# Performance work log

Measured on AMD Instinct MI355X. Metric: run time of the kernel, lower is better.

Reference implementation:

```python
import jax, jax.numpy as jnp
import numpy as np

FEAT_STRIDE = 16
PRE_NMS_TOPN = 6000
POST_NMS_TOPN = 300
NMS_THRESH = 0.7
NEG = -1e9  # sentinel for suppressed scores


def generate_anchors(base_size=16, ratios=np.array([0.5, 1.0, 2.0]), scales=np.array([8.0, 16.0, 32.0])):
    ctr = (base_size - 1) / 2.0
    size = float(base_size * base_size)
    ws_r = np.round(np.sqrt(size / ratios))
    hs_r = np.round(ws_r * ratios)
    ws = (ws_r[:, None] * scales[None, :]).reshape(-1)
    hs = (hs_r[:, None] * scales[None, :]).reshape(-1)
    return np.stack([ctr - 0.5 * (ws - 1), ctr - 0.5 * (hs - 1),
                     ctr + 0.5 * (ws - 1), ctr + 0.5 * (hs - 1)], axis=1).astype(np.float32)

ANCHORS = jnp.asarray(generate_anchors())  # [A, 4]


def bbox_transform_inv(anchors, deltas):
    # anchors [N,4], deltas [B,N,4] -> [B,N,4]
    w = anchors[:, 2] - anchors[:, 0] + 1.0
    h = anchors[:, 3] - anchors[:, 1] + 1.0
    cx = anchors[:, 0] + 0.5 * w
    cy = anchors[:, 1] + 0.5 * h
    dx, dy, dw, dh = deltas[..., 0], deltas[..., 1], deltas[..., 2], deltas[..., 3]
    pcx = dx * w + cx
    pcy = dy * h + cy
    pw = jnp.exp(dw) * w
    ph = jnp.exp(dh) * h
    return jnp.stack([pcx - 0.5 * pw, pcy - 0.5 * ph, pcx + 0.5 * pw, pcy + 0.5 * ph], axis=-1)


def nms_single(boxes, scores):
    # Greedy NMS on pre-sorted candidates; boxes [N,4], scores [N].
    areas = (boxes[:, 2] - boxes[:, 0] + 1.0) * (boxes[:, 3] - boxes[:, 1] + 1.0)

    def body(sc, _):
        i = jnp.argmax(sc)
        valid = sc[i] > NEG / 2
        b = boxes[i]
        xx1 = jnp.maximum(b[0], boxes[:, 0])
        yy1 = jnp.maximum(b[1], boxes[:, 1])
        xx2 = jnp.minimum(b[2], boxes[:, 2])
        yy2 = jnp.minimum(b[3], boxes[:, 3])
        inter = jnp.maximum(xx2 - xx1 + 1.0, 0.0) * jnp.maximum(yy2 - yy1 + 1.0, 0.0)
        iou = inter / (areas[i] + areas - inter)
        sc = jnp.where(iou > NMS_THRESH, NEG, sc)  # suppress (includes self, iou=1)
        return sc, (i, valid)

    _, (keep, valid) = jax.lax.scan(body, scores, None, length=POST_NMS_TOPN)
    kept_boxes = jnp.where(valid[:, None], boxes[keep], 0.0)  # pad rows -> zeros
    return kept_boxes


def reference(scores, bbox_deltas, im_info):
    B, _, H, W = scores.shape
    A = ANCHORS.shape[0]
    # fg probs: second set of A channels -> [B, K*A]
    fg = jnp.transpose(scores[:, A:, :, :], (0, 2, 3, 1)).reshape(B, -1)
    deltas = jnp.transpose(bbox_deltas, (0, 2, 3, 1)).reshape(B, -1, 4)

    # Shifted anchors over the feature grid: [K*A, 4]
    sx = jnp.arange(W, dtype=jnp.float32) * FEAT_STRIDE
    sy = jnp.arange(H, dtype=jnp.float32) * FEAT_STRIDE
    mx, my = jnp.meshgrid(sx, sy)  # [H, W]
    shifts = jnp.stack([mx.ravel(), my.ravel(), mx.ravel(), my.ravel()], axis=1)  # [K,4]
    anchors = (ANCHORS[None, :, :] + shifts[:, None, :]).reshape(-1, 4)

    proposals = bbox_transform_inv(anchors, deltas)  # [B, K*A, 4]

    # Clip to image per batch element (im_info = [height, width, scale])
    wmax = (im_info[:, 1] - 1.0)[:, None]
    hmax = (im_info[:, 0] - 1.0)[:, None]
    proposals = jnp.stack([
        jnp.clip(proposals[..., 0], 0.0, wmax),
        jnp.clip(proposals[..., 1], 0.0, hmax),
        jnp.clip(proposals[..., 2], 0.0, wmax),
        jnp.clip(proposals[..., 3], 0.0, hmax)], axis=-1)

    # Top pre_nms_topN by score (sorted descending)
    top_scores, top_idx = jax.lax.top_k(fg, PRE_NMS_TOPN)            # [B, pre]
    top_boxes = jnp.take_along_axis(proposals, top_idx[..., None], axis=1)  # [B, pre, 4]

    kept = jax.vmap(nms_single)(top_boxes, top_scores)  # [B, post, 4]

    batch_col = jnp.broadcast_to(
        jnp.arange(B, dtype=kept.dtype)[:, None, None], (B, POST_NMS_TOPN, 1))
    return jnp.concatenate([batch_col, kept], axis=-1)  # [B, post, 5]


def setup_inputs() -> dict:
    key = jax.random.key(0)
    k1, k2 = jax.random.split(key)
    B, A, H, W = 16, 9, 192, 192
    scores = jax.random.uniform(k1, (B, 2 * A, H, W), dtype=jnp.float32)
    bbox_deltas = jax.random.normal(k2, (B, 4 * A, H, W), dtype=jnp.float32) * 0.5
    im_info = jnp.tile(jnp.array([[H * 16.0, W * 16.0, 1.0]], dtype=jnp.float32), (B, 1))
    return {"scores": scores, "bbox_deltas": bbox_deltas, "im_info": im_info}
```

## Files before the change

kernel.cpp:

```cpp
#include <hip/hip_runtime.h>
#include <stdint.h>

#define A_NUM    9
#define W_FEAT   192
#define H_FEAT   192
#define K_FEAT   (W_FEAT * H_FEAT)
#define N_ANCH   (K_FEAT * A_NUM)
#define BATCH    16
#define PRE_NMS  6000
#define POST_NMS 300
#define CAP      8192
#define CHUNK    4096
#define BPB      (N_ANCH / CHUNK)
#define CPA      (K_FEAT / CHUNK)
#define SORT2    2048
#define NWORD    (SORT2 / 64)
#define SLOTS    64

#define T2KEY    0xBF7Fu

typedef unsigned long long u64;

__constant__ float c_anchors[A_NUM][4] = {
    { -84.f,  -40.f,  99.f,  55.f},
    {-176.f,  -88.f, 191.f, 103.f},
    {-360.f, -184.f, 375.f, 199.f},
    { -56.f,  -56.f,  71.f,  71.f},
    {-120.f, -120.f, 135.f, 135.f},
    {-248.f, -248.f, 263.f, 263.f},
    { -36.f,  -80.f,  51.f,  95.f},
    { -80.f, -168.f,  95.f, 183.f},
    {-168.f, -344.f, 183.f, 359.f},
};

__device__ __forceinline__ unsigned key_bits(float s) {
    unsigned ub = __float_as_uint(s);
    return (ub & 0x80000000u) ? ~ub : (ub | 0x80000000u);
}

__device__ __forceinline__ const float* chunk_ptr(const float* scores, int blk,
                                                  int& b, int& a, int& koff) {
    b = blk / BPB;
    int chunk = blk - b * BPB;
    a = chunk / CPA;
    koff = (chunk - a * CPA) * CHUNK;
    return scores + ((size_t)(b * 2 * A_NUM + A_NUM + a)) * K_FEAT + koff;
}

__device__ __forceinline__ void hist_add(unsigned* lh, unsigned bin) {
    unsigned long long peers = __ballot(1);
// ... 18 lines not shown
    float dh = deltas[dbase + (size_t)3 * K_FEAT];
    float ax1 = c_anchors[a][0] + ww * 16.0f;
    float ay1 = c_anchors[a][1] + hh * 16.0f;
    float ax2 = c_anchors[a][2] + ww * 16.0f;
    float ay2 = c_anchors[a][3] + hh * 16.0f;
    float waf = ax2 - ax1 + 1.0f, haf = ay2 - ay1 + 1.0f;
    float cx = ax1 + 0.5f * waf, cy = ay1 + 0.5f * haf;
    float pcx = dx * waf + cx, pcy = dy * haf + cy;
    float pw = expf(dw) * waf, ph = expf(dh) * haf;
    float4 box;
    box.x = fminf(fmaxf(pcx - 0.5f * pw, 0.f), wmax);
    box.y = fminf(fmaxf(pcy - 0.5f * ph, 0.f), hmax);
    box.z = fminf(fmaxf(pcx + 0.5f * pw, 0.f), wmax);
    box.w = fminf(fmaxf(pcy + 0.5f * ph, 0.f), hmax);
    return box;
}

__device__ __forceinline__ bool iou_over(float4 a, float aa, float4 c, float ca) {
    float xx1 = fmaxf(a.x, c.x), yy1 = fmaxf(a.y, c.y);
    float xx2 = fminf(a.z, c.z), yy2 = fminf(a.w, c.w);
    float iw = fmaxf(xx2 - xx1 + 1.f, 0.f);
    float ih = fmaxf(yy2 - yy1 + 1.f, 0.f);
    float inter = iw * ih;
    return inter > 0.7f * (aa + ca - inter);
}

__device__ __forceinline__ u64 shflxor64(u64 v, int j) {
    unsigned lo = (unsigned)v, hi = (unsigned)(v >> 32);
    lo = __shfl_xor(lo, j, 64);
    hi = __shfl_xor(hi, j, 64);
    return ((u64)hi << 32) | lo;
}

__global__ __launch_bounds__(256) void compact_kernel(
        const float* __restrict__ scores,
        unsigned* __restrict__ cnt_blk,
        u64* __restrict__ cand) {
    __shared__ u64 sbuf[256];
    __shared__ unsigned scount;
    int tid = threadIdx.x;
    if (tid == 0) scount = 0;
    __syncthreads();
    int b, a, koff;
    const float* p = chunk_ptr(scores, blockIdx.x, b, a, koff);
    const float4* p4 = (const float4*)p;
    #pragma unroll
    for (int it = 0; it < CHUNK / 1024; ++it) {
        float4 v = p4[it * 256 + tid];
        unsigned e0 = (unsigned)(koff + (it * 256 + tid) * 4);
        float vv[4] = {v.x, v.y, v.z, v.w};
        #pragma unroll
        for (int j = 0; j < 4; ++j) {
            unsigned ub = key_bits(vv[j]);
            if ((ub >> 16) >= T2KEY) {
                unsigned n = (e0 + j) * A_NUM + a;
                unsigned pos = atomicAdd(&scount, 1u);
                if (pos < 256)
                    sbuf[pos] = ((u64)ub << 32) | (unsigned)(~n);
            }
        }
    }
    __syncthreads();
    unsigned c = scount;
    if (tid == 0) cnt_blk[blockIdx.x] = c;
    unsigned cw = c < SLOTS ? c : SLOTS;
    if (tid < cw) cand[(size_t)blockIdx.x * SLOTS + tid] = sbuf[tid];
}

#define KEYRD(I)  ((((u64)khi[(I)]) << 32) | klo[(I)])
#define KEYWR(I, V) do { khi[(I)] = (unsigned)((V) >> 32); klo[(I)] = (unsigned)(V); } while (0)

#define CE_SHFL(E, J, DESC) do { \
    u64 _v = shflxor64((E), (J)); \
    bool _kmax = ((DESC) == ((l & (J)) == 0)); \
    (E) = _kmax ? ((E) > _v ? (E) : _v) : ((E) < _v ? (E) : _v); \
} while (0)

#define CE_PAIR(A, B, DESC) do { \
    u64 _mx = (A) > (B) ? (A) : (B); \
    u64 _mn = (A) > (B) ? (B) : (A); \
    if (DESC) { (A) = _mx; (B) = _mn; } else { (A) = _mn; (B) = _mx; } \
} while (0)

#define LDS_PHASE(K, J) do { \
    _Pragma("unroll") \
    for (int pp = 0; pp < 2; ++pp) { \
        unsigned p = (unsigned)tid + (unsigned)pp * 512u; \
        unsigned i = ((p & ~((unsigned)(J) - 1u)) << 1) | (p & ((unsigned)(J) - 1u)); \
        unsigned ixj = i | (unsigned)(J); \
        u64 x = KEYRD(i), y = KEYRD(ixj); \
        bool dsc = ((i & (unsigned)(K)) == 0u); \
        if (dsc ? (x < y) : (x > y)) { KEYWR(i, y); KEYWR(ixj, x); } \
    } \
    __syncthreads(); \
} while (0)

#define REG_TAIL(D) do { \
    int seg = w << 8; \
    bool d = (D); \
    u64 e0 = KEYRD(seg + l); \
    u64 e1 = KEYRD(seg + 64 + l); \
    u64 e2 = KEYRD(seg + 128 + l); \
    u64 e3 = KEYRD(seg + 192 + l); \
    CE_PAIR(e0, e2, d); CE_PAIR(e1, e3, d); \
    CE_PAIR(e0, e1, d); CE_PAIR(e2, e3, d); \
    _Pragma("unroll") \
    for (int j = 32; j >= 1; j >>= 1) { \
        CE_SHFL(e0, j, d); CE_SHFL(e1, j, d); \
        CE_SHFL(e2, j, d); CE_SHFL(e3, j, d); \
    } \
    KEYWR(seg + l, e0); KEYWR(seg + 64 + l, e1); \
    KEYWR(seg + 128 + l, e2); KEYWR(seg + 192 + l, e3); \
    __syncthreads(); \
} while (0)

__global__ __launch_bounds__(512) void sort_kernel(
        const unsigned* __restrict__ cnt_blk,
        const u64* __restrict__ cand,
        const float* __restrict__ deltas,
        const float* __restrict__ im_info,
        float4* __restrict__ bxg,
        unsigned* __restrict__ m2arr,
        unsigned* __restrict__ okarr) {
    int b = blockIdx.x;
    __shared__ unsigned khi[SORT2];
    __shared__ unsigned klo[SORT2];
    __shared__ unsigned offs[BPB + 1];
    __shared__ unsigned ovfl;
    int tid = threadIdx.x;
    int l = tid & 63, w = tid >> 6;

    if (tid == 0) { ovfl = 0; offs[0] = 0; }
    __syncthreads();
    if (tid < BPB) {
        unsigned c = cnt_blk[b * BPB + tid];
        if (c > SLOTS) atomicOr(&ovfl, 1u);
        offs[tid + 1] = (c > SLOTS) ? SLOTS : c;
    }
    for (int i = tid; i < SORT2; i += 512) { khi[i] = 0u; klo[i] = 0u; }
    __syncthreads();
    if (tid == 0)
        for (int i = 1; i <= BPB; ++i) offs[i] += offs[i - 1];
    __syncthreads();
    unsigned m2 = offs[BPB];
    bool ok = (!ovfl) && (m2 >= 1) && (m2 <= SORT2);

    if (ok) {
        for (int s = w; s < BPB; s += 8) {
            unsigned c = offs[s + 1] - offs[s];
            if ((unsigned)l < c) {
                u64 k = cand[(size_t)(b * BPB + s) * SLOTS + l];
                KEYWR(offs[s] + l, k);
            }
        }
    }
    __syncthreads();

    if (ok) {
        {
            int seg = w << 8;
            u64 e0 = KEYRD(seg + l);
            u64 e1 = KEYRD(seg + 64 + l);
            u64 e2 = KEYRD(seg + 128 + l);
            u64 e3 = KEYRD(seg + 192 + l);
            #pragma unroll
            for (int k = 2; k <= 32; k <<= 1) {
                bool d = ((l & k) == 0);
                #pragma unroll
                for (int j = k >> 1; j >= 1; j >>= 1) {
                    CE_SHFL(e0, j, d); CE_SHFL(e1, j, d);
                    CE_SHFL(e2, j, d); CE_SHFL(e3, j, d);
                }
            }
            #pragma unroll
            for (int j = 32; j >= 1; j >>= 1) {
                CE_SHFL(e0, j, true);  CE_SHFL(e1, j, false);
                CE_SHFL(e2, j, true);  CE_SHFL(e3, j, false);
            }
            CE_PAIR(e0, e1, true); CE_PAIR(e2, e3, false);
            #pragma unroll
            for (int j = 32; j >= 1; j >>= 1) {
                CE_SHFL(e0, j, true);  CE_SHFL(e1, j, true);
                CE_SHFL(e2, j, false); CE_SHFL(e3, j, false);
            }
            {
                bool d = ((w & 1) == 0);
                CE_PAIR(e0, e2, d); CE_PAIR(e1, e3, d);
                CE_PAIR(e0, e1, d); CE_PAIR(e2, e3, d);
                #pragma unroll
                for (int j = 32; j >= 1; j >>= 1) {
                    CE_SHFL(e0, j, d); CE_SHFL(e1, j, d);
                    CE_SHFL(e2, j, d); CE_SHFL(e3, j, d);
                }
            }
            KEYWR(seg + l, e0); KEYWR(seg + 64 + l, e1);
            KEYWR(seg + 128 + l, e2); KEYWR(seg + 192 + l, e3);
        }
        __syncthreads();
        LDS_PHASE(512, 256);                 REG_TAIL(((w & 2) == 0));
        LDS_PHASE(1024, 512); LDS_PHASE(1024, 256);  REG_TAIL(((w & 4) == 0));
        LDS_PHASE(2048, 1024); LDS_PHASE(2048, 512); LDS_PHASE(2048, 256);
        REG_TAIL(true);

        float wmax = im_info[b * 3 + 1] - 1.0f;
        float hmax = im_info[b * 3 + 0] - 1.0f;
        int mceil = (int)((m2 + 63u) & ~63u);
        for (int i = tid; i < mceil; i += 512) {
            float4 v;
            if (i < (int)m2) v = decode_box(~klo[i], deltas, b, wmax, hmax);
            else             v = make_float4(-3e9f, -3e9f, -3e9f, -3e9f);
            bxg[(size_t)b * SORT2 + i] = v;
        }
    }
    if (tid == 0) { m2arr[b] = m2; okarr[b] = ok ? 1u : 0u; }
}

__global__ __launch_bounds__(256) void mask_kernel(
        const float4* __restrict__ bxg,
        const unsigned* __restrict__ m2arr,
        const unsigned* __restrict__ okarr,
        u64* __restrict__ mask) {
    int b = blockIdx.x >> 5;
    int t = blockIdx.x & 31;
    if (!okarr[b]) return;
    unsigned m2 = m2arr[b];
    if ((unsigned)(t * 64) >= m2) return;
    __shared__ float4 sb[SORT2];
    __shared__ float  sa[SORT2];
    int tid = threadIdx.x;
    int mceil = (int)((m2 + 63u) & ~63u);
    for (int i = tid; i < mceil; i += 256) {
        float4 v = bxg[(size_t)b * SORT2 + i];
        sb[i] = v;
        sa[i] = (v.z - v.x + 1.f) * (v.w - v.y + 1.f);
    }
    __syncthreads();
    int r = t * 64 + (tid >> 2);
    int q = tid & 3;
    float4 rb = sb[r];
    float  ra = sa[r];
    u64* mrow = mask + ((size_t)b * SORT2 + r) * NWORD;
    for (int w = t + q; w < NWORD; w += 4) {
        if (w * 64 >= mceil) break;
        u64 bits = 0;
        #pragma unroll 4
        for (int jj = 0; jj < 64; ++jj) {
            int j = w * 64 + jj;
            bits |= ((u64)(iou_over(rb, ra, sb[j], sa[j]) ? 1 : 0)) << jj;
        }
        mrow[w] = bits;
    }
}

__global__ __launch_bounds__(512) void resolve_fb_kernel(
        const float4* __restrict__ bxg,
        const u64* __restrict__ mask,
        const unsigned* __restrict__ m2arr,
        const unsigned* __restrict__ okarr,
        const float* __restrict__ scores,
        const float* __restrict__ deltas,
        const float* __restrict__ im_info,
        float4* __restrict__ fbbox,
        float* __restrict__ out) {
    int b = blockIdx.x;
    int tid = threadIdx.x;
    __shared__ unsigned short kept_idx[POST_NMS];
    __shared__ unsigned nk_sh;
    __shared__ unsigned lh[256];
    __shared__ unsigned d8_sh, above_sh, tbin_sh, fbcnt;
    __shared__ u64 keys[CAP];

    bool okb = (okarr[b] != 0);
    if (tid == 0) nk_sh = 0;
    __syncthreads();

    if (okb && tid < 64) {
        int lane = tid;
        int m2 = (int)m2arr[b];
        const u64* mb = mask + (size_t)b * SORT2 * NWORD;
        u64 S = 0;
        int w32 = lane & 31;
        bool hiHalf = lane >= 32;
        int nchunks = (m2 + 63) >> 6;
        u64 dpre = mb[(size_t)lane * NWORD + 0];
        int nk = 0;
        for (int c = 0; c < nchunks && nk < POST_NMS; ++c) {
            int base = c * 64;
            int nvalid = min(64, m2 - base);
            u64 d = dpre;
            if (c + 1 < nchunks)
                dpre = mb[(size_t)(base + 64 + lane) * NWORD + (c + 1)];
            unsigned wl0 = __builtin_amdgcn_readlane((unsigned)S, c);
            unsigned wh0 = __builtin_amdgcn_readlane((unsigned)(S >> 32), c);
            unsigned wl1 = __builtin_amdgcn_readlane((unsigned)S, c + 32);
            unsigned wh1 = __builtin_amdgcn_readlane((unsigned)(S >> 32), c + 32);
            u64 Sc = (((u64)wh0 << 32) | wl0) | (((u64)wh1 << 32) | wl1);
            u64 live = ~Sc;
            if (nvalid < 64) live &= (1ull << nvalid) - 1ull;
            u64 keptC = 0;
            while (live && nk < POST_NMS) {
                int il = (int)__ffsll((long long)live) - 1;
                unsigned dlo = __builtin_amdgcn_readlane((unsigned)d, il);
                unsigned dhi = __builtin_amdgcn_readlane((unsigned)(d >> 32), il);
                u64 drow = ((u64)dhi << 32) | dlo;
                live &= ~drow;
                live &= ~(1ull << il);
                if (lane == 0) kept_idx[nk] = (unsigned short)(base + il);
                keptC |= 1ull << il;
                ++nk;
            }
            if (nk < POST_NMS && c + 1 < nchunks && keptC) {
                long long kc = (long long)keptC;
                while (kc) {
                    int r0  = (int)__ffsll(kc) - 1; kc &= kc - 1;
                    int r1  = (int)__ffsll(kc) - 1; kc &= kc - 1;
                    int r2  = (int)__ffsll(kc) - 1; kc &= kc - 1;
                    int r3  = (int)__ffsll(kc) - 1; kc &= kc - 1;
                    int r4  = (int)__ffsll(kc) - 1; kc &= kc - 1;
                    int r5  = (int)__ffsll(kc) - 1; kc &= kc - 1;
                    int r6  = (int)__ffsll(kc) - 1; kc &= kc - 1;
                    int r7  = (int)__ffsll(kc) - 1; kc &= kc - 1;
                    int r8  = (int)__ffsll(kc) - 1; kc &= kc - 1;
                    int r9  = (int)__ffsll(kc) - 1; kc &= kc - 1;
                    int r10 = (int)__ffsll(kc) - 1; kc &= kc - 1;
                    int r11 = (int)__ffsll(kc) - 1; kc &= kc - 1;
                    int r12 = (int)__ffsll(kc) - 1; kc &= kc - 1;
                    int r13 = (int)__ffsll(kc) - 1; kc &= kc - 1;
                    int r14 = (int)__ffsll(kc) - 1; kc &= kc - 1;
                    int r15 = (int)__ffsll(kc) - 1; kc &= kc - 1;
                    int s0 = hiHalf ? r1  : r0;
                    int s1 = hiHalf ? r3  : r2;
                    int s2 = hiHalf ? r5  : r4;
                    int s3 = hiHalf ? r7  : r6;
                    int s4 = hiHalf ? r9  : r8;
                    int s5 = hiHalf ? r11 : r10;
                    int s6 = hiHalf ? r13 : r12;
                    int s7 = hiHalf ? r15 : r14;
                    u64 a0 = 0, a1 = 0, a2 = 0, a3 = 0;
                    u64 a4 = 0, a5 = 0, a6 = 0, a7 = 0;
                    if (s0 >= 0) a0 = mb[(size_t)(base + s0) * NWORD + w32];
                    if (s1 >= 0) a1 = mb[(size_t)(base + s1) * NWORD + w32];
                    if (s2 >= 0) a2 = mb[(size_t)(base + s2) * NWORD + w32];
                    if (s3 >= 0) a3 = mb[(size_t)(base + s3) * NWORD + w32];
                    if (s4 >= 0) a4 = mb[(size_t)(base + s4) * NWORD + w32];
                    if (s5 >= 0) a5 = mb[(size_t)(base + s5) * NWORD + w32];
                    if (s6 >= 0) a6 = mb[(size_t)(base + s6) * NWORD + w32];
                    if (s7 >= 0) a7 = mb[(size_t)(base + s7) * NWORD + w32];
                    S |= (a0 | a1) | (a2 | a3) | (a4 | a5) | (a6 | a7);
                }
            }
        }
        if (lane == 0) nk_sh = (unsigned)nk;
    }
    __syncthreads();

    unsigned nk = nk_sh;
    bool ok_final = okb && (nk == POST_NMS);
    if (ok_final) {
        const float4* bx = bxg + (size_t)b * SORT2;
        for (int t = tid; t < POST_NMS; t += 512) {
            float4 kb = bx[kept_idx[t]];
            float* o = out + ((size_t)b * POST_NMS + t) * 5;
            o[0] = (float)b;
            o[1] = kb.x; o[2] = kb.y; o[3] = kb.z; o[4] = kb.w;
        }
        return;
    }

    if (tid < 256) lh[tid] = 0;
    __syncthreads();
    for (int a = 0; a < A_NUM; ++a) {
        const float* p = scores + ((size_t)(b * 2 * A_NUM + A_NUM + a)) * K_FEAT;
        for (int k = tid; k < K_FEAT; k += 512)
            hist_add(lh, key_bits(p[k]) >> 24);
    }
    __syncthreads();
    if (tid == 0) {
        unsigned acc = 0; int d = 0;
        for (int i = 255; i >= 0; --i) {
            unsigned v = lh[i];
            if (acc + v >= PRE_NMS) { d = i; break; }
            acc += v;
        }
        d8_sh = (unsigned)d; above_sh = acc;
    }
    __syncthreads();
    unsigned dd = d8_sh;
    if (tid < 256) lh[tid] = 0;
    __syncthreads();
    for (int a = 0; a < A_NUM; ++a) {
        const float* p = scores + ((size_t)(b * 2 * A_NUM + A_NUM + a)) * K_FEAT;
        for (int k = tid; k < K_FEAT; k += 512) {
            unsigned u = key_bits(p[k]);
            if ((u >> 24) == dd) hist_add(lh, (u >> 16) & 0xFF);
        }
    }
    __syncthreads();
    if (tid == 0) {
        unsigned acc = above_sh; int d = 0;
        for (int i = 255; i >= 0; --i) {
            unsigned v = lh[i];
            if (acc + v >= PRE_NMS) { d = i; break; }
            acc += v;
        }
        tbin_sh = (dd << 8) | (unsigned)d;
        fbcnt = 0;
    }
    __syncthreads();
    unsigned tb = tbin_sh;
    for (int i = tid; i < CAP; i += 512) keys[i] = 0ULL;
    __syncthreads();
    for (int a = 0; a < A_NUM; ++a) {
        const float* p = scores + ((size_t)(b * 2 * A_NUM + A_NUM + a)) * K_FEAT;
        for (int k = tid; k < K_FEAT; k += 512) {
            unsigned u = key_bits(p[k]);
            if ((u >> 16) >= tb) {
                unsigned n = (unsigned)k * A_NUM + (unsigned)a;
                unsigned pos = atomicAdd(&fbcnt, 1u);
                if (pos < CAP) keys[pos] = ((u64)u << 32) | (unsigned)(~n);
            }
        }
    }
    __syncthreads();
    for (unsigned k = 2; k <= CAP; k <<= 1) {
        for (unsigned j = k >> 1; j > 0; j >>= 1) {
            #pragma unroll
            for (int pp = 0; pp < 8; ++pp) {
                unsigned p = (unsigned)tid + (unsigned)pp * 512u;
                unsigned i = ((p & ~(j - 1)) << 1) | (p & (j - 1));
                unsigned ixj = i | j;
                u64 x = keys[i], y = keys[ixj];
                bool desc = ((i & k) == 0);
                if (desc ? (x < y) : (x > y)) { keys[i] = y; keys[ixj] = x; }
            }
            __syncthreads();
        }
    }
    float wmax = im_info[b * 3 + 1] - 1.0f;
    float hmax = im_info[b * 3 + 0] - 1.0f;
    for (int i = tid; i < PRE_NMS; i += 512) {
        unsigned n = ~(unsigned)(keys[i] & 0xFFFFFFFFull);
        float4 box = make_float4(0.f, 0.f, 0.f, 0.f);
        if (n < N_ANCH) box = decode_box(n, deltas, b, wmax, hmax);
        fbbox[(size_t)b * PRE_NMS + i] = box;
    }
    __syncthreads();
    if (tid >= 64) return;
    int lane = tid;
    float4 k0, k1v, k2v, k3v, k4v;
    float a0 = 1.f, a1 = 1.f, a2 = 1.f, a3 = 1.f, a4 = 1.f;
    k0 = k1v = k2v = k3v = k4v = make_float4(0.f, 0.f, 0.f, 0.f);
    const float4* bb = fbbox + (size_t)b * PRE_NMS;
    int nk2 = 0;
    for (int i = 0; i < PRE_NMS && nk2 < POST_NMS; ++i) {
        float4 cur = bb[i];
        float ca = (cur.z - cur.x + 1.f) * (cur.w - cur.y + 1.f);
        bool s = false;
        if (nk2 > 0)   { bool v = lane < nk2;       s |= v && iou_over(k0,  a0, cur, ca); }
        if (nk2 > 64)  { bool v = 64 + lane < nk2;  s |= v && iou_over(k1v, a1, cur, ca); }
        if (nk2 > 128) { bool v = 128 + lane < nk2; s |= v && iou_over(k2v, a2, cur, ca); }
        if (nk2 > 192) { bool v = 192 + lane < nk2; s |= v && iou_over(k3v, a3, cur, ca); }
        if (nk2 > 256) { bool v = 256 + lane < nk2; s |= v && iou_over(k4v, a4, cur, ca); }
        if (!__any(s)) {
            int r = nk2 >> 6;
            if (lane == (nk2 & 63)) {
                if      (r == 0) { k0  = cur; a0 = ca; }
                else if (r == 1) { k1v = cur; a1 = ca; }
                else if (r == 2) { k2v = cur; a2 = ca; }
                else if (r == 3) { k3v = cur; a3 = ca; }
                else             { k4v = cur; a4 = ca; }
            }
            if (lane == 0) {
                float* o = out + ((size_t)b * POST_NMS + nk2) * 5;
                o[0] = (float)b;
                o[1] = cur.x; o[2] = cur.y; o[3] = cur.z; o[4] = cur.w;
            }
            ++nk2;
        }
    }
    for (int t = nk2 + lane; t < POST_NMS; t += 64) {
        float* o = out + ((size_t)b * POST_NMS + t) * 5;
        o[0] = (float)b;
        o[1] = 0.f; o[2] = 0.f; o[3] = 0.f; o[4] = 0.f;
    }
}

extern "C" void kernel_launch(void* const* d_in, const int* in_sizes, int n_in,
                              void* d_out, int out_size, void* d_ws, size_t ws_size,
                              hipStream_t stream) {
    const float* scores  = (const float*)d_in[0];
    const float* deltas  = (const float*)d_in[1];
    const float* im_info = (const float*)d_in[2];
    float* out = (float*)d_out;

    size_t off = 0;
    unsigned* cnt_blk = (unsigned*)((char*)d_ws + off);
    off += (size_t)BATCH * BPB * 4;
    off = (off + 255) & ~(size_t)255;
    u64* cand = (u64*)((char*)d_ws + off);
    off += (size_t)BATCH * BPB * SLOTS * 8;
    off = (off + 255) & ~(size_t)255;
    unsigned* m2arr = (unsigned*)((char*)d_ws + off);
    off += (size_t)BATCH * 4;
    off = (off + 255) & ~(size_t)255;
    unsigned* okarr = (unsigned*)((char*)d_ws + off);
    off += (size_t)BATCH * 4;
    off = (off + 255) & ~(size_t)255;
    float4* bxg = (float4*)((char*)d_ws + off);
    off += (size_t)BATCH * SORT2 * 16;
    off = (off + 255) & ~(size_t)255;
    u64* mask = (u64*)((char*)d_ws + off);
    off += (size_t)BATCH * SORT2 * NWORD * 8;
    off = (off + 255) & ~(size_t)255;
    float4* fbbox = (float4*)((char*)d_ws + off);

    compact_kernel   <<<BATCH * BPB, 256, 0, stream>>>(scores, cnt_blk, cand);
    sort_kernel      <<<BATCH, 512, 0, stream>>>(cnt_blk, cand, deltas, im_info,
                                                 bxg, m2arr, okarr);
    mask_kernel      <<<BATCH * 32, 256, 0, stream>>>(bxg, m2arr, okarr, mask);
    resolve_fb_kernel<<<BATCH, 512, 0, stream>>>(bxg, mask, m2arr, okarr,
                                                 scores, deltas, im_info,
                                                 fbbox, out);
}
```

Before: 105.9 us.

## Fuse four pipeline kernels into one cooperative kernel with grid syncs

Replaces the compact, sort, mask and resolve launches with a single cooperative kernel of 256 blocks of 512 threads, separated by grid.sync barriers. Stages reuse a shared-memory union. The compact stage loops over chunks with a grid stride, and the mask stage is repartitioned to 16 blocks per batch covering 128 rows each, skipping lower-triangle words. The goal is to remove launch overheads and inter-kernel gaps, at the cost of grid-sync latency, large static LDS limiting occupancy, and idle blocks during the single-block-per-batch sort and resolve stages.

Result: slower. 178.2 us (+68.3%).

```diff
diff --git a/kernel.cpp b/kernel.cpp
--- a/kernel.cpp
+++ b/kernel.cpp
@@ -1,5 +1,8 @@
 #include <hip/hip_runtime.h>
+#include <hip/hip_cooperative_groups.h>
 #include <stdint.h>
+
+namespace cg = cooperative_groups;
 
 #define A_NUM    9
 #define W_FEAT   192
@@ -16,6 +19,7 @@
 #define SORT2    2048
 #define NWORD    (SORT2 / 64)
 #define SLOTS    64
+#define GRID     256
 
 #define T2KEY    0xBF7Fu
 
@@ -100,41 +104,6 @@
     return ((u64)hi << 32) | lo;
 }
 
-__global__ __launch_bounds__(256) void compact_kernel(
-        const float* __restrict__ scores,
-        unsigned* __restrict__ cnt_blk,
-        u64* __restrict__ cand) {
-    __shared__ u64 sbuf[256];
-    __shared__ unsigned scount;
-    int tid = threadIdx.x;
-    if (tid == 0) scount = 0;
-    __syncthreads();
-    int b, a, koff;
-    const float* p = chunk_ptr(scores, blockIdx.x, b, a, koff);
-    const float4* p4 = (const float4*)p;
-    #pragma unroll
-    for (int it = 0; it < CHUNK / 1024; ++it) {
-        float4 v = p4[it * 256 + tid];
-        unsigned e0 = (unsigned)(koff + (it * 256 + tid) * 4);
-        float vv[4] = {v.x, v.y, v.z, v.w};
-        #pragma unroll
-        for (int j = 0; j < 4; ++j) {
-            unsigned ub = key_bits(vv[j]);
-            if ((ub >> 16) >= T2KEY) {
-                unsigned n = (e0 + j) * A_NUM + a;
-                unsigned pos = atomicAdd(&scount, 1u);
-                if (pos < 256)
-                    sbuf[pos] = ((u64)ub << 32) | (unsigned)(~n);
-            }
-        }
-    }
-    __syncthreads();
-    unsigned c = scount;
-    if (tid == 0) cnt_blk[blockIdx.x] = c;
-    unsigned cw = c < SLOTS ? c : SLOTS;
-    if (tid < cw) cand[(size_t)blockIdx.x * SLOTS + tid] = sbuf[tid];
-}
-
 #define KEYRD(I)  ((((u64)khi[(I)]) << 32) | klo[(I)])
 #define KEYWR(I, V) do { khi[(I)] = (unsigned)((V) >> 32); klo[(I)] = (unsigned)(V); } while (0)
 
@@ -182,374 +151,407 @@
     __syncthreads(); \
 } while (0)
 
-__global__ __launch_bounds__(512) void sort_kernel(
-        const unsigned* __restrict__ cnt_blk,
-        const u64* __restrict__ cand,
-        const float* __restrict__ deltas,
-        const float* __restrict__ im_info,
-        float4* __restrict__ bxg,
-        unsigned* __restrict__ m2arr,
-        unsigned* __restrict__ okarr) {
-    int b = blockIdx.x;
-    __shared__ unsigned khi[SORT2];
-    __shared__ unsigned klo[SORT2];
-    __shared__ unsigned offs[BPB + 1];
-    __shared__ unsigned ovfl;
-    int tid = threadIdx.x;
-    int l = tid & 63, w = tid >> 6;
-
-    if (tid == 0) { ovfl = 0; offs[0] = 0; }
-    __syncthreads();
-    if (tid < BPB) {
-        unsigned c = cnt_blk[b * BPB + tid];
-        if (c > SLOTS) atomicOr(&ovfl, 1u);
-        offs[tid + 1] = (c > SLOTS) ? SLOTS : c;
-    }
-    for (int i = tid; i < SORT2; i += 512) { khi[i] = 0u; klo[i] = 0u; }
-    __syncthreads();
-    if (tid == 0)
-        for (int i = 1; i <= BPB; ++i) offs[i] += offs[i - 1];
-    __syncthreads();
-    unsigned m2 = offs[BPB];
-    bool ok = (!ovfl) && (m2 >= 1) && (m2 <= SORT2);
-
-    if (ok) {
-        for (int s = w; s < BPB; s += 8) {
-            unsigned c = offs[s + 1] - offs[s];
-            if ((unsigned)l < c) {
-                u64 k = cand[(size_t)(b * BPB + s) * SLOTS + l];
-                KEYWR(offs[s] + l, k);
-            }
-        }
-    }
-    __syncthreads();
-
-    if (ok) {
-        {
-            int seg = w << 8;
-            u64 e0 = KEYRD(seg + l);
-            u64 e1 = KEYRD(seg + 64 + l);
-            u64 e2 = KEYRD(seg + 128 + l);
-            u64 e3 = KEYRD(seg + 192 + l);
-            #pragma unroll
-            for (int k = 2; k <= 32; k <<= 1) {
-                bool d = ((l & k) == 0);
-                #pragma unroll
-                for (int j = k >> 1; j >= 1; j >>= 1) {
-                    CE_SHFL(e0, j, d); CE_SHFL(e1, j, d);
-                    CE_SHFL(e2, j, d); CE_SHFL(e3, j, d);
-                }
-            }
-            #pragma unroll
-            for (int j = 32; j >= 1; j >>= 1) {
-                CE_SHFL(e0, j, true);  CE_SHFL(e1, j, false);
-                CE_SHFL(e2, j, true);  CE_SHFL(e3, j, false);
-            }
-            CE_PAIR(e0, e1, true); CE_PAIR(e2, e3, false);
-            #pragma unroll
-            for (int j = 32; j >= 1; j >>= 1) {
-                CE_SHFL(e0, j, true);  CE_SHFL(e1, j, true);
-                CE_SHFL(e2, j, false); CE_SHFL(e3, j, false);
-            }
-            {
-                bool d = ((w & 1) == 0);
-                CE_PAIR(e0, e2, d); CE_PAIR(e1, e3, d);
-                CE_PAIR(e0, e1, d); CE_PAIR(e2, e3, d);
-                #pragma unroll
-                for (int j = 32; j >= 1; j >>= 1) {
-                    CE_SHFL(e0, j, d); CE_SHFL(e1, j, d);
-                    CE_SHFL(e2, j, d); CE_SHFL(e3, j, d);
-                }
-            }
-            KEYWR(seg + l, e0); KEYWR(seg + 64 + l, e1);
-            KEYWR(seg + 128 + l, e2); KEYWR(seg + 192 + l, e3);
-        }
-        __syncthreads();
-        LDS_PHASE(512, 256);                 REG_TAIL(((w & 2) == 0));
-        LDS_PHASE(1024, 512); LDS_PHASE(1024, 256);  REG_TAIL(((w & 4) == 0));
-        LDS_PHASE(2048, 1024); LDS_PHASE(2048, 512); LDS_PHASE(2048, 256);
-        REG_TAIL(true);
-
-        float wmax = im_info[b * 3 + 1] - 1.0f;
-        float hmax = im_info[b * 3 + 0] - 1.0f;
-        int mceil = (int)((m2 + 63u) & ~63u);
-        for (int i = tid; i < mceil; i += 512) {
-            float4 v;
-            if (i < (int)m2) v = decode_box(~klo[i], deltas, b, wmax, hmax);
-            else             v = make_float4(-3e9f, -3e9f, -3e9f, -3e9f);
-            bxg[(size_t)b * SORT2 + i] = v;
-        }
-    }
-    if (tid == 0) { m2arr[b] = m2; okarr[b] = ok ? 1u : 0u; }
-}
-
-__global__ __launch_bounds__(256) void mask_kernel(
-        const float4* __restrict__ bxg,
-        const unsigned* __restrict__ m2arr,
-        const unsigned* __restrict__ okarr,
-        u64* __restrict__ mask) {
-    int b = blockIdx.x >> 5;
-    int t = blockIdx.x & 31;
-    if (!okarr[b]) return;
-    unsigned m2 = m2arr[b];
-    if ((unsigned)(t * 64) >= m2) return;
-    __shared__ float4 sb[SORT2];
-    __shared__ float  sa[SORT2];
-    int tid = threadIdx.x;
-    int mceil = (int)((m2 + 63u) & ~63u);
-    for (int i = tid; i < mceil; i += 256) {
-        float4 v = bxg[(size_t)b * SORT2 + i];
-        sb[i] = v;
-        sa[i] = (v.z - v.x + 1.f) * (v.w - v.y + 1.f);
-    }
-    __syncthreads();
-    int r = t * 64 + (tid >> 2);
-    int q = tid & 3;
-    float4 rb = sb[r];
-    float  ra = sa[r];
-    u64* mrow = mask + ((size_t)b * SORT2 + r) * NWORD;
-    for (int w = t + q; w < NWORD; w += 4) {
-        if (w * 64 >= mceil) break;
-        u64 bits = 0;
-        #pragma unroll 4
-        for (int jj = 0; jj < 64; ++jj) {
-            int j = w * 64 + jj;
-            bits |= ((u64)(iou_over(rb, ra, sb[j], sa[j]) ? 1 : 0)) << jj;
-        }
-        mrow[w] = bits;
-    }
-}
-
-__global__ __launch_bounds__(512) void resolve_fb_kernel(
-        const float4* __restrict__ bxg,
-        const u64* __restrict__ mask,
-        const unsigned* __restrict__ m2arr,
-        const unsigned* __restrict__ okarr,
+__global__ __launch_bounds__(512) void giga_kernel(
         const float* __restrict__ scores,
         const float* __restrict__ deltas,
         const float* __restrict__ im_info,
+        unsigned* __restrict__ cnt_blk,
+        u64* __restrict__ cand,
+        float4* __restrict__ bxg,
+        unsigned* __restrict__ m2arr,
+        unsigned* __restrict__ okarr,
+        u64* __restrict__ mask,
         float4* __restrict__ fbbox,
         float* __restrict__ out) {
-    int b = blockIdx.x;
+    cg::grid_group grid = cg::this_grid();
     int tid = threadIdx.x;
+    int l = tid & 63, w = tid >> 6;
+
+    __shared__ __align__(16) char smemA[65536];
+    __shared__ __align__(16) char smemB[8192];
+    __shared__ unsigned offs[BPB + 1];
     __shared__ unsigned short kept_idx[POST_NMS];
-    __shared__ unsigned nk_sh;
-    __shared__ unsigned lh[256];
+    __shared__ unsigned sc0, ovfl, nk_sh;
     __shared__ unsigned d8_sh, above_sh, tbin_sh, fbcnt;
-    __shared__ u64 keys[CAP];
-
-    bool okb = (okarr[b] != 0);
-    if (tid == 0) nk_sh = 0;
-    __syncthreads();
-
-    if (okb && tid < 64) {
+
+    {
+        u64* sbuf = (u64*)smemA;
+        for (int blk = blockIdx.x; blk < BATCH * BPB; blk += GRID) {
+            if (tid == 0) sc0 = 0;
+            __syncthreads();
+            int b, a, koff;
+            const float* p = chunk_ptr(scores, blk, b, a, koff);
+            const float4* p4 = (const float4*)p;
+            #pragma unroll
+            for (int it = 0; it < CHUNK / 2048; ++it) {
+                float4 v = p4[it * 512 + tid];
+                unsigned e0 = (unsigned)(koff + (it * 512 + tid) * 4);
+                float vv[4] = {v.x, v.y, v.z, v.w};
+                #pragma unroll
+                for (int j = 0; j < 4; ++j) {
+                    unsigned ub = key_bits(vv[j]);
+                    if ((ub >> 16) >= T2KEY) {
+                        unsigned n = (e0 + j) * A_NUM + a;
+                        unsigned pos = atomicAdd(&sc0, 1u);
+                        if (pos < 256)
+                            sbuf[pos] = ((u64)ub << 32) | (unsigned)(~n);
+                    }
+                }
+            }
+            __syncthreads();
+            unsigned c = sc0;
+            if (tid == 0) cnt_blk[blk] = c;
+            unsigned cw = c < SLOTS ? c : SLOTS;
+            if (tid < (int)cw) cand[(size_t)blk * SLOTS + tid] = sbuf[tid];
+            __syncthreads();
+        }
+    }
+    grid.sync();
+
+    if (blockIdx.x < BATCH) {
+        int b = blockIdx.x;
+        unsigned* khi = (unsigned*)smemA;
+        unsigned* klo = khi + SORT2;
+        if (tid == 0) { ovfl = 0; offs[0] = 0; }
+        __syncthreads();
+        if (tid < BPB) {
+            unsigned c = cnt_blk[b * BPB + tid];
+            if (c > SLOTS) atomicOr(&ovfl, 1u);
+            offs[tid + 1] = (c > SLOTS) ? SLOTS : c;
+        }
+        for (int i = tid; i < SORT2; i += 512) { khi[i] = 0u; klo[i] = 0u; }
+        __syncthreads();
+        if (tid == 0)
+            for (int i = 1; i <= BPB; ++i) offs[i] += offs[i - 1];
+        __syncthreads();
+        unsigned m2 = offs[BPB];
+        bool ok = (!ovfl) && (m2 >= 1) && (m2 <= SORT2);
+
+        if (ok) {
+            for (int s = w; s < BPB; s += 8) {
+                unsigned c = offs[s + 1] - offs[s];
+                if ((unsigned)l < c) {
+                    u64 k = cand[(size_t)(b * BPB + s) * SLOTS + l];
+                    KEYWR(offs[s] + l, k);
+                }
+            }
+        }
+        __syncthreads();
+
+        if (ok) {
+            {
+                int seg = w << 8;
+                u64 e0 = KEYRD(seg + l);
+                u64 e1 = KEYRD(seg + 64 + l);
+                u64 e2 = KEYRD(seg + 128 + l);
+                u64 e3 = KEYRD(seg + 192 + l);
+                #pragma unroll
+                for (int k = 2; k <= 32; k <<= 1) {
+                    bool d = ((l & k) == 0);
+                    #pragma unroll
+                    for (int j = k >> 1; j >= 1; j >>= 1) {
+                        CE_SHFL(e0, j, d); CE_SHFL(e1, j, d);
+                        CE_SHFL(e2, j, d); CE_SHFL(e3, j, d);
+                    }
+                }
+                #pragma unroll
+                for (int j = 32; j >= 1; j >>= 1) {
+                    CE_SHFL(e0, j, true);  CE_SHFL(e1, j, false);
+                    CE_SHFL(e2, j, true);  CE_SHFL(e3, j, false);
+                }
+                CE_PAIR(e0, e1, true); CE_PAIR(e2, e3, false);
+                #pragma unroll
+                for (int j = 32; j >= 1; j >>= 1) {
+                    CE_SHFL(e0, j, true);  CE_SHFL(e1, j, true);
+                    CE_SHFL(e2, j, false); CE_SHFL(e3, j, false);
+                }
+                {
+                    bool d = ((w & 1) == 0);
+                    CE_PAIR(e0, e2, d); CE_PAIR(e1, e3, d);
+                    CE_PAIR(e0, e1, d); CE_PAIR(e2, e3, d);
+                    #pragma unroll
+                    for (int j = 32; j >= 1; j >>= 1) {
+                        CE_SHFL(e0, j, d); CE_SHFL(e1, j, d);
+                        CE_SHFL(e2, j, d); CE_SHFL(e3, j, d);
+                    }
+                }
+                KEYWR(seg + l, e0); KEYWR(seg + 64 + l, e1);
+                KEYWR(seg + 128 + l, e2); KEYWR(seg + 192 + l, e3);
+            }
+            __syncthreads();
+            LDS_PHASE(512, 256);                 REG_TAIL(((w & 2) == 0));
+            LDS_PHASE(1024, 512); LDS_PHASE(1024, 256);  REG_TAIL(((w & 4) == 0));
+            LDS_PHASE(2048, 1024); LDS_PHASE(2048, 512); LDS_PHASE(2048, 256);
+            REG_TAIL(true);
+
+            float wmax = im_info[b * 3 + 1] - 1.0f;
+            float hmax = im_info[b * 3 + 0] - 1.0f;
+            int mceil = (int)((m2 + 63u) & ~63u);
+            for (int i = tid; i < mceil; i += 512) {
+                float4 v;
+                if (i < (int)m2) v = decode_box(~klo[i], deltas, b, wmax, hmax);
+                else             v = make_float4(-3e9f, -3e9f, -3e9f, -3e9f);
+                bxg[(size_t)b * SORT2 + i] = v;
+            }
+        }
+        if (tid == 0) { m2arr[b] = m2; okarr[b] = ok ? 1u : 0u; }
+    }
+    grid.sync();
+
+    {
+        int mb_ = blockIdx.x >> 4;
+        int t = blockIdx.x & 15;
+        unsigned m2 = m2arr[mb_];
+        bool okb = (okarr[mb_] != 0);
+        int mceil = (int)((m2 + 63u) & ~63u);
+        if (okb && t * 128 < mceil) {
+            float4* sb = (float4*)smemA;
+            float*  sa = (float*)smemB;
+            for (int i = tid; i < mceil; i += 512) {
+                float4 v = bxg[(size_t)mb_ * SORT2 + i];
+                sb[i] = v;
+                sa[i] = (v.z - v.x + 1.f) * (v.w - v.y + 1.f);
+            }
+            __syncthreads();
+            int r = t * 128 + (tid >> 2);
+            int q = tid & 3;
+            int nw = mceil >> 6;
+            if (r < mceil) {
+                float4 rb = sb[r];
+                float  ra = sa[r];
+                u64* mrow = mask + ((size_t)mb_ * SORT2 + r) * NWORD;
+                for (int w_ = (r >> 6) + q; w_ < nw; w_ += 4) {
+                    u64 bits = 0;
+                    #pragma unroll 4
+                    for (int jj = 0; jj < 64; ++jj) {
+                        int j = w_ * 64 + jj;
+                        bits |= ((u64)(iou_over(rb, ra, sb[j], sa[j]) ? 1 : 0)) << jj;
+                    }
+                    mrow[w_] = bits;
+                }
+            }
+        }
+    }
+    grid.sync();
+
+    if (blockIdx.x >= BATCH) return;
+    {
+        int b = blockIdx.x;
+        bool okb = (okarr[b] != 0);
+        if (tid == 0) nk_sh = 0;
+        __syncthreads();
+
+        if (okb && tid < 64) {
+            int lane = tid;
+            int m2 = (int)m2arr[b];
+            const u64* mb = mask + (size_t)b * SORT2 * NWORD;
+            u64 S = 0;
+            int w32 = lane & 31;
+            bool hiHalf = lane >= 32;
+            int nchunks = (m2 + 63) >> 6;
+            u64 dpre = mb[(size_t)lane * NWORD + 0];
+            int nk = 0;
+            for (int c = 0; c < nchunks && nk < POST_NMS; ++c) {
+                int base = c * 64;
+                int nvalid = min(64, m2 - base);
+                u64 d = dpre;
+                if (c + 1 < nchunks)
+                    dpre = mb[(size_t)(base + 64 + lane) * NWORD + (c + 1)];
+                unsigned wl0 = __builtin_amdgcn_readlane((unsigned)S, c);
+                unsigned wh0 = __builtin_amdgcn_readlane((unsigned)(S >> 32), c);
+                unsigned wl1 = __builtin_amdgcn_readlane((unsigned)S, c + 32);
+                unsigned wh1 = __builtin_amdgcn_readlane((unsigned)(S >> 32), c + 32);
+                u64 Sc = (((u64)wh0 << 32) | wl0) | (((u64)wh1 << 32) | wl1);
+                u64 live = ~Sc;
+                if (nvalid < 64) live &= (1ull << nvalid) - 1ull;
+                u64 keptC = 0;
+                while (live && nk < POST_NMS) {
+                    int il = (int)__ffsll((long long)live) - 1;
+                    unsigned dlo = __builtin_amdgcn_readlane((unsigned)d, il);
+                    unsigned dhi = __builtin_amdgcn_readlane((unsigned)(d >> 32), il);
+                    u64 drow = ((u64)dhi << 32) | dlo;
+                    live &= ~drow;
+                    live &= ~(1ull << il);
+                    if (lane == 0) kept_idx[nk] = (unsigned short)(base + il);
+                    keptC |= 1ull << il;
+                    ++nk;
+                }
+                if (nk < POST_NMS && c + 1 < nchunks && keptC) {
+                    long long kc = (long long)keptC;
+                    while (kc) {
+                        int r0  = (int)__ffsll(kc) - 1; kc &= kc - 1;
+                        int r1  = (int)__ffsll(kc) - 1; kc &= kc - 1;
+                        int r2  = (int)__ffsll(kc) - 1; kc &= kc - 1;
+                        int r3  = (int)__ffsll(kc) - 1; kc &= kc - 1;
+                        int r4  = (int)__ffsll(kc) - 1; kc &= kc - 1;
+                        int r5  = (int)__ffsll(kc) - 1; kc &= kc - 1;
+                        int r6  = (int)__ffsll(kc) - 1; kc &= kc - 1;
+                        int r7  = (int)__ffsll(kc) - 1; kc &= kc - 1;
+                        int r8  = (int)__ffsll(kc) - 1; kc &= kc - 1;
+                        int r9  = (int)__ffsll(kc) - 1; kc &= kc - 1;
+                        int r10 = (int)__ffsll(kc) - 1; kc &= kc - 1;
+                        int r11 = (int)__ffsll(kc) - 1; kc &= kc - 1;
+                        int r12 = (int)__ffsll(kc) - 1; kc &= kc - 1;
+                        int r13 = (int)__ffsll(kc) - 1; kc &= kc - 1;
+                        int r14 = (int)__ffsll(kc) - 1; kc &= kc - 1;
+                        int r15 = (int)__ffsll(kc) - 1; kc &= kc - 1;
+                        int s0 = hiHalf ? r1  : r0;
+                        int s1 = hiHalf ? r3  : r2;
+                        int s2 = hiHalf ? r5  : r4;
+                        int s3 = hiHalf ? r7  : r6;
+                        int s4 = hiHalf ? r9  : r8;
+                        int s5 = hiHalf ? r11 : r10;
+                        int s6 = hiHalf ? r13 : r12;
+                        int s7 = hiHalf ? r15 : r14;
+                        u64 a0 = 0, a1 = 0, a2 = 0, a3 = 0;
+                        u64 a4 = 0, a5 = 0, a6 = 0, a7 = 0;
+                        if (s0 >= 0) a0 = mb[(size_t)(base + s0) * NWORD + w32];
+                        if (s1 >= 0) a1 = mb[(size_t)(base + s1) * NWORD + w32];
+                        if (s2 >= 0) a2 = mb[(size_t)(base + s2) * NWORD + w32];
+                        if (s3 >= 0) a3 = mb[(size_t)(base + s3) * NWORD + w32];
+                        if (s4 >= 0) a4 = mb[(size_t)(base + s4) * NWORD + w32];
+                        if (s5 >= 0) a5 = mb[(size_t)(base + s5) * NWORD + w32];
+                        if (s6 >= 0) a6 = mb[(size_t)(base + s6) * NWORD + w32];
+                        if (s7 >= 0) a7 = mb[(size_t)(base + s7) * NWORD + w32];
+                        S |= (a0 | a1) | (a2 | a3) | (a4 | a5) | (a6 | a7);
+                    }
+                }
+            }
+            if (lane == 0) nk_sh = (unsigned)nk;
+        }
+        __syncthreads();
+
+        unsigned nk = nk_sh;
+        bool ok_final = okb && (nk == POST_NMS);
+        if (ok_final) {
+            const float4* bx = bxg + (size_t)b * SORT2;
+            for (int t = tid; t < POST_NMS; t += 512) {
+                float4 kb = bx[kept_idx[t]];
+                float* o = out + ((size_t)b * POST_NMS + t) * 5;
+                o[0] = (float)b;
+                o[1] = kb.x; o[2] = kb.y; o[3] = kb.z; o[4] = kb.w;
+            }
+            return;
+        }
+
+        u64* keys = (u64*)smemA;
+        unsigned* lh = (unsigned*)smemB;
+        if (tid < 256) lh[tid] = 0;
+        __syncthreads();
+        for (int a = 0; a < A_NUM; ++a) {
+            const float* p = scores + ((size_t)(b * 2 * A_NUM + A_NUM + a)) * K_FEAT;
+            for (int k = tid; k < K_FEAT; k += 512)
+                hist_add(lh, key_bits(p[k]) >> 24);
+        }
+        __syncthreads();
+        if (tid == 0) {
+            unsigned acc = 0; int d = 0;
+            for (int i = 255; i >= 0; --i) {
+                unsigned v = lh[i];
+                if (acc + v >= PRE_NMS) { d = i; break; }
+                acc += v;
+            }
+            d8_sh = (unsigned)d; above_sh = acc;
+        }
+        __syncthreads();
+        unsigned dd = d8_sh;
+        if (tid < 256) lh[tid] = 0;
+        __syncthreads();
+        for (int a = 0; a < A_NUM; ++a) {
+            const float* p = scores + ((size_t)(b * 2 * A_NUM + A_NUM + a)) * K_FEAT;
+            for (int k = tid; k < K_FEAT; k += 512) {
+                unsigned u = key_bits(p[k]);
+                if ((u >> 24) == dd) hist_add(lh, (u >> 16) & 0xFF);
+            }
+        }
+        __syncthreads();
+        if (tid == 0) {
+            unsigned acc = above_sh; int d = 0;
+            for (int i = 255; i >= 0; --i) {
+                unsigned v = lh[i];
+                if (acc + v >= PRE_NMS) { d = i; break; }
+                acc += v;
+            }
+            tbin_sh = (dd << 8) | (unsigned)d;
+            fbcnt = 0;
+        }
+        __syncthreads();
+        unsigned tb = tbin_sh;
+        for (int i = tid; i < CAP; i += 512) keys[i] = 0ULL;
+        __syncthreads();
+        for (int a = 0; a < A_NUM; ++a) {
+            const float* p = scores + ((size_t)(b * 2 * A_NUM + A_NUM + a)) * K_FEAT;
+            for (int k = tid; k < K_FEAT; k += 512) {
+                unsigned u = key_bits(p[k]);
+                if ((u >> 16) >= tb) {
+                    unsigned n = (unsigned)k * A_NUM + (unsigned)a;
+                    unsigned pos = atomicAdd(&fbcnt, 1u);
+                    if (pos < CAP) keys[pos] = ((u64)u << 32) | (unsigned)(~n);
+                }
+            }
+        }
+        __syncthreads();
+        for (unsigned k = 2; k <= CAP; k <<= 1) {
+            for (unsigned j = k >> 1; j > 0; j >>= 1) {
+                #pragma unroll
+                for (int pp = 0; pp < 8; ++pp) {
+                    unsigned p = (unsigned)tid + (unsigned)pp * 512u;
+                    unsigned i = ((p & ~(j - 1)) << 1) | (p & (j - 1));
+                    unsigned ixj = i | j;
+                    u64 x = keys[i], y = keys[ixj];
+                    bool desc = ((i & k) == 0);
+                    if (desc ? (x < y) : (x > y)) { keys[i] = y; keys[ixj] = x; }
+                }
+                __syncthreads();
+            }
+        }
+        float wmax = im_info[b * 3 + 1] - 1.0f;
+        float hmax = im_info[b * 3 + 0] - 1.0f;
+        for (int i = tid; i < PRE_NMS; i += 512) {
+            unsigned n = ~(unsigned)(keys[i] & 0xFFFFFFFFull);
+            float4 box = make_float4(0.f, 0.f, 0.f, 0.f);
+            if (n < N_ANCH) box = decode_box(n, deltas, b, wmax, hmax);
+            fbbox[(size_t)b * PRE_NMS + i] = box;
+        }
+        __syncthreads();
+        if (tid >= 64) return;
         int lane = tid;
-        int m2 = (int)m2arr[b];
-        const u64* mb = mask + (size_t)b * SORT2 * NWORD;
-        u64 S = 0;
-        int w32 = lane & 31;
-        bool hiHalf = lane >= 32;
-        int nchunks = (m2 + 63) >> 6;
-        u64 dpre = mb[(size_t)lane * NWORD + 0];
-        int nk = 0;
-        for (int c = 0; c < nchunks && nk < POST_NMS; ++c) {
-            int base = c * 64;
-            int nvalid = min(64, m2 - base);
-            u64 d = dpre;
-            if (c + 1 < nchunks)
-                dpre = mb[(size_t)(base + 64 + lane) * NWORD + (c + 1)];
-            unsigned wl0 = __builtin_amdgcn_readlane((unsigned)S, c);
-            unsigned wh0 = __builtin_amdgcn_readlane((unsigned)(S >> 32), c);
-            unsigned wl1 = __builtin_amdgcn_readlane((unsigned)S, c + 32);
-            unsigned wh1 = __builtin_amdgcn_readlane((unsigned)(S >> 32), c + 32);
-            u64 Sc = (((u64)wh0 << 32) | wl0) | (((u64)wh1 << 32) | wl1);
-            u64 live = ~Sc;
-            if (nvalid < 64) live &= (1ull << nvalid) - 1ull;
-            u64 keptC = 0;
-            while (live && nk < POST_NMS) {
-                int il = (int)__ffsll((long long)live) - 1;
-                unsigned dlo = __builtin_amdgcn_readlane((unsigned)d, il);
-                unsigned dhi = __builtin_amdgcn_readlane((unsigned)(d >> 32), il);
-                u64 drow = ((u64)dhi << 32) | dlo;
-                live &= ~drow;
-                live &= ~(1ull << il);
-                if (lane == 0) kept_idx[nk] = (unsigned short)(base + il);
-                keptC |= 1ull << il;
-                ++nk;
-            }
-            if (nk < POST_NMS && c + 1 < nchunks && keptC) {
-                long long kc = (long long)keptC;
-                while (kc) {
-                    int r0  = (int)__ffsll(kc) - 1; kc &= kc - 1;
-                    int r1  = (int)__ffsll(kc) - 1; kc &= kc - 1;
-                    int r2  = (int)__ffsll(kc) - 1; kc &= kc - 1;
-                    int r3  = (int)__ffsll(kc) - 1; kc &= kc - 1;
-                    int r4  = (int)__ffsll(kc) - 1; kc &= kc - 1;
-                    int r5  = (int)__ffsll(kc) - 1; kc &= kc - 1;
-                    int r6  = (int)__ffsll(kc) - 1; kc &= kc - 1;
-                    int r7  = (int)__ffsll(kc) - 1; kc &= kc - 1;
-                    int r8  = (int)__ffsll(kc) - 1; kc &= kc - 1;
-                    int r9  = (int)__ffsll(kc) - 1; kc &= kc - 1;
-                    int r10 = (int)__ffsll(kc) - 1; kc &= kc - 1;
-                    int r11 = (int)__ffsll(kc) - 1; kc &= kc - 1;
-                    int r12 = (int)__ffsll(kc) - 1; kc &= kc - 1;
-                    int r13 = (int)__ffsll(kc) - 1; kc &= kc - 1;
-                    int r14 = (int)__ffsll(kc) - 1; kc &= kc - 1;
-                    int r15 = (int)__ffsll(kc) - 1; kc &= kc - 1;
-                    int s0 = hiHalf ? r1  : r0;
-                    int s1 = hiHalf ? r3  : r2;
-                    int s2 = hiHalf ? r5  : r4;
-                    int s3 = hiHalf ? r7  : r6;
-                    int s4 = hiHalf ? r9  : r8;
-                    int s5 = hiHalf ? r11 : r10;
-                    int s6 = hiHalf ? r13 : r12;
-                    int s7 = hiHalf ? r15 : r14;
-                    u64 a0 = 0, a1 = 0, a2 = 0, a3 = 0;
-                    u64 a4 = 0, a5 = 0, a6 = 0, a7 = 0;
-                    if (s0 >= 0) a0 = mb[(size_t)(base + s0) * NWORD + w32];
-                    if (s1 >= 0) a1 = mb[(size_t)(base + s1) * NWORD + w32];
-                    if (s2 >= 0) a2 = mb[(size_t)(base + s2) * NWORD + w32];
-                    if (s3 >= 0) a3 = mb[(size_t)(base + s3) * NWORD + w32];
-                    if (s4 >= 0) a4 = mb[(size_t)(base + s4) * NWORD + w32];
-                    if (s5 >= 0) a5 = mb[(size_t)(base + s5) * NWORD + w32];
-                    if (s6 >= 0) a6 = mb[(size_t)(base + s6) * NWORD + w32];
-                    if (s7 >= 0) a7 = mb[(size_t)(base + s7) * NWORD + w32];
-                    S |= (a0 | a1) | (a2 | a3) | (a4 | a5) | (a6 | a7);
-                }
-            }
-        }
-        if (lane == 0) nk_sh = (unsigned)nk;
-    }
-    __syncthreads();
-
-    unsigned nk = nk_sh;
-    bool ok_final = okb && (nk == POST_NMS);
-    if (ok_final) {
-        const float4* bx = bxg + (size_t)b * SORT2;
-        for (int t = tid; t < POST_NMS; t += 512) {
-            float4 kb = bx[kept_idx[t]];
+        float4 k0, k1v, k2v, k3v, k4v;
+        float a0 = 1.f, a1 = 1.f, a2 = 1.f, a3 = 1.f, a4 = 1.f;
+        k0 = k1v = k2v = k3v = k4v = make_float4(0.f, 0.f, 0.f, 0.f);
+        const float4* bb = fbbox + (size_t)b * PRE_NMS;
+        int nk2 = 0;
+        for (int i = 0; i < PRE_NMS && nk2 < POST_NMS; ++i) {
+            float4 cur = bb[i];
+            float ca = (cur.z - cur.x + 1.f) * (cur.w - cur.y + 1.f);
+            bool s = false;
+            if (nk2 > 0)   { bool v = lane < nk2;       s |= v && iou_over(k0,  a0, cur, ca); }
+            if (nk2 > 64)  { bool v = 64 + lane < nk2;  s |= v && iou_over(k1v, a1, cur, ca); }
+            if (nk2 > 128) { bool v = 128 + lane < nk2; s |= v && iou_over(k2v, a2, cur, ca); }
+            if (nk2 > 192) { bool v = 192 + lane < nk2; s |= v && iou_over(k3v, a3, cur, ca); }
+            if (nk2 > 256) { bool v = 256 + lane < nk2; s |= v && iou_over(k4v, a4, cur, ca); }
+            if (!__any(s)) {
+                int r = nk2 >> 6;
+                if (lane == (nk2 & 63)) {
+                    if      (r == 0) { k0  = cur; a0 = ca; }
+                    else if (r == 1) { k1v = cur; a1 = ca; }
+                    else if (r == 2) { k2v = cur; a2 = ca; }
+                    else if (r == 3) { k3v = cur; a3 = ca; }
+                    else             { k4v = cur; a4 = ca; }
+                }
+                if (lane == 0) {
+                    float* o = out + ((size_t)b * POST_NMS + nk2) * 5;
+                    o[0] = (float)b;
+                    o[1] = cur.x; o[2] = cur.y; o[3] = cur.z; o[4] = cur.w;
+                }
+                ++nk2;
+            }
+        }
+        for (int t = nk2 + lane; t < POST_NMS; t += 64) {
             float* o = out + ((size_t)b * POST_NMS + t) * 5;
             o[0] = (float)b;
-            o[1] = kb.x; o[2] = kb.y; o[3] = kb.z; o[4] = kb.w;
-        }
-        return;
-    }
-
-    if (tid < 256) lh[tid] = 0;
-    __syncthreads();
-    for (int a = 0; a < A_NUM; ++a) {
-        const float* p = scores + ((size_t)(b * 2 * A_NUM + A_NUM + a)) * K_FEAT;
-        for (int k = tid; k < K_FEAT; k += 512)
-            hist_add(lh, key_bits(p[k]) >> 24);
-    }
-    __syncthreads();
-    if (tid == 0) {
-        unsigned acc = 0; int d = 0;
-        for (int i = 255; i >= 0; --i) {
-            unsigned v = lh[i];
-            if (acc + v >= PRE_NMS) { d = i; break; }
-            acc += v;
-        }
-        d8_sh = (unsigned)d; above_sh = acc;
-    }
-    __syncthreads();
-    unsigned dd = d8_sh;
-    if (tid < 256) lh[tid] = 0;
-    __syncthreads();
-    for (int a = 0; a < A_NUM; ++a) {
-        const float* p = scores + ((size_t)(b * 2 * A_NUM + A_NUM + a)) * K_FEAT;
-        for (int k = tid; k < K_FEAT; k += 512) {
-            unsigned u = key_bits(p[k]);
-            if ((u >> 24) == dd) hist_add(lh, (u >> 16) & 0xFF);
-        }
-    }
-    __syncthreads();
-    if (tid == 0) {
-        unsigned acc = above_sh; int d = 0;
-        for (int i = 255; i >= 0; --i) {
-            unsigned v = lh[i];
-            if (acc + v >= PRE_NMS) { d = i; break; }
-            acc += v;
-        }
-        tbin_sh = (dd << 8) | (unsigned)d;
-        fbcnt = 0;
-    }
-    __syncthreads();
-    unsigned tb = tbin_sh;
-    for (int i = tid; i < CAP; i += 512) keys[i] = 0ULL;
-    __syncthreads();
-    for (int a = 0; a < A_NUM; ++a) {
-        const float* p = scores + ((size_t)(b * 2 * A_NUM + A_NUM + a)) * K_FEAT;
-        for (int k = tid; k < K_FEAT; k += 512) {
-            unsigned u = key_bits(p[k]);
-            if ((u >> 16) >= tb) {
-                unsigned n = (unsigned)k * A_NUM + (unsigned)a;
-                unsigned pos = atomicAdd(&fbcnt, 1u);
-                if (pos < CAP) keys[pos] = ((u64)u << 32) | (unsigned)(~n);
-            }
-        }
-    }
-    __syncthreads();
-    for (unsigned k = 2; k <= CAP; k <<= 1) {
-        for (unsigned j = k >> 1; j > 0; j >>= 1) {
-            #pragma unroll
-            for (int pp = 0; pp < 8; ++pp) {
-                unsigned p = (unsigned)tid + (unsigned)pp * 512u;
-                unsigned i = ((p & ~(j - 1)) << 1) | (p & (j - 1));
-                unsigned ixj = i | j;
-                u64 x = keys[i], y = keys[ixj];
-                bool desc = ((i & k) == 0);
-                if (desc ? (x < y) : (x > y)) { keys[i] = y; keys[ixj] = x; }
-            }
-            __syncthreads();
-        }
-    }
-    float wmax = im_info[b * 3 + 1] - 1.0f;
-    float hmax = im_info[b * 3 + 0] - 1.0f;
-    for (int i = tid; i < PRE_NMS; i += 512) {
-        unsigned n = ~(unsigned)(keys[i] & 0xFFFFFFFFull);
-        float4 box = make_float4(0.f, 0.f, 0.f, 0.f);
-        if (n < N_ANCH) box = decode_box(n, deltas, b, wmax, hmax);
-        fbbox[(size_t)b * PRE_NMS + i] = box;
-    }
-    __syncthreads();
-    if (tid >= 64) return;
-    int lane = tid;
-    float4 k0, k1v, k2v, k3v, k4v;
-    float a0 = 1.f, a1 = 1.f, a2 = 1.f, a3 = 1.f, a4 = 1.f;
-    k0 = k1v = k2v = k3v = k4v = make_float4(0.f, 0.f, 0.f, 0.f);
-    const float4* bb = fbbox + (size_t)b * PRE_NMS;
-    int nk2 = 0;
-    for (int i = 0; i < PRE_NMS && nk2 < POST_NMS; ++i) {
-        float4 cur = bb[i];
-        float ca = (cur.z - cur.x + 1.f) * (cur.w - cur.y + 1.f);
-        bool s = false;
-        if (nk2 > 0)   { bool v = lane < nk2;       s |= v && iou_over(k0,  a0, cur, ca); }
-        if (nk2 > 64)  { bool v = 64 + lane < nk2;  s |= v && iou_over(k1v, a1, cur, ca); }
-        if (nk2 > 128) { bool v = 128 + lane < nk2; s |= v && iou_over(k2v, a2, cur, ca); }
-        if (nk2 > 192) { bool v = 192 + lane < nk2; s |= v && iou_over(k3v, a3, cur, ca); }
-        if (nk2 > 256) { bool v = 256 + lane < nk2; s |= v && iou_over(k4v, a4, cur, ca); }
-        if (!__any(s)) {
-            int r = nk2 >> 6;
-            if (lane == (nk2 & 63)) {
-                if      (r == 0) { k0  = cur; a0 = ca; }
-                else if (r == 1) { k1v = cur; a1 = ca; }
-                else if (r == 2) { k2v = cur; a2 = ca; }
-                else if (r == 3) { k3v = cur; a3 = ca; }
-                else             { k4v = cur; a4 = ca; }
-            }
-            if (lane == 0) {
-                float* o = out + ((size_t)b * POST_NMS + nk2) * 5;
-                o[0] = (float)b;
-                o[1] = cur.x; o[2] = cur.y; o[3] = cur.z; o[4] = cur.w;
-            }
-            ++nk2;
-        }
-    }
-    for (int t = nk2 + lane; t < POST_NMS; t += 64) {
-        float* o = out + ((size_t)b * POST_NMS + t) * 5;
-        o[0] = (float)b;
-        o[1] = 0.f; o[2] = 0.f; o[3] = 0.f; o[4] = 0.f;
+            o[1] = 0.f; o[2] = 0.f; o[3] = 0.f; o[4] = 0.f;
+        }
     }
 }
 
@@ -582,11 +584,12 @@
     off = (off + 255) & ~(size_t)255;
     float4* fbbox = (float4*)((char*)d_ws + off);
 
-    compact_kernel   <<<BATCH * BPB, 256, 0, stream>>>(scores, cnt_blk, cand);
-    sort_kernel      <<<BATCH, 512, 0, stream>>>(cnt_blk, cand, deltas, im_info,
-                                                 bxg, m2arr, okarr);
-    mask_kernel      <<<BATCH * 32, 256, 0, stream>>>(bxg, m2arr, okarr, mask);
-    resolve_fb_kernel<<<BATCH, 512, 0, stream>>>(bxg, mask, m2arr, okarr,
-                                                 scores, deltas, im_info,
-                                                 fbbox, out);
-}
+    void* args[] = {
+        (void*)&scores, (void*)&deltas, (void*)&im_info,
+        (void*)&cnt_blk, (void*)&cand, (void*)&bxg,
+        (void*)&m2arr, (void*)&okarr, (void*)&mask,
+        (void*)&fbbox, (void*)&out
+    };
+    hipLaunchCooperativeKernel((void*)giga_kernel, dim3(GRID), dim3(512),
+                               args, 0, stream);
+}
```
